# Kernel optimization log

Hardware: AMD Instinct MI355X
Metric: run time of the kernel (lower is better)

The kernel has to match this reference:

```python
import jax, jax.numpy as jnp
import numpy as np

B, CIN, H, W = 8, 64, 128, 128
COUT, K = 64, 3
STRIDE, PAD, DIL, G = 1, 1, 1, 1
T = K * K
HO = (H + 2 * PAD - (DIL * (K - 1) + 1)) // STRIDE + 1
WO = (W + 2 * PAD - (DIL * (K - 1) + 1)) // STRIDE + 1


def setup_inputs() -> dict:
    key = jax.random.key(0)
    ks = jax.random.split(key, 5)
    x = jax.random.normal(ks[0], (B, CIN, H, W), jnp.float32)
    offset = jax.random.normal(ks[1], (B, 2 * G * T, HO, WO), jnp.float32)
    mask = jax.random.uniform(ks[2], (B, G * T, HO, WO), jnp.float32)
    weight = jax.random.normal(ks[3], (COUT, CIN, K, K), jnp.float32) * (1.0 / np.sqrt(CIN * T))
    bias = jnp.zeros((COUT,), jnp.float32)
    return {"x": x, "offset": offset, "mask": mask, "weight": weight, "bias": bias}


def _gather(img_f, idx):
    # img_f: [Cg, H*W], idx: [T, Ho, Wo] -> [Cg, T, Ho, Wo]
    return img_f[:, idx]


def _dcn(x, offset, mask, weight, bias):
    Bn, Cin, Hh, Ww = x.shape
    Cout = weight.shape[0]
    Cg = Cin // G
    # offset channels laid out as [G, T, (dy, dx)] per DCNv2 convention
    off = offset.reshape(Bn, G, T, 2, HO, WO)
    dy, dx = off[:, :, :, 0], off[:, :, :, 1]  # [B, G, T, Ho, Wo]
    ky, kx = jnp.meshgrid(jnp.arange(K), jnp.arange(K), indexing="ij")
    ky = (ky.reshape(T) * DIL).astype(jnp.float32)
    kx = (kx.reshape(T) * DIL).astype(jnp.float32)
    base_y = (jnp.arange(HO) * STRIDE - PAD).astype(jnp.float32)
    base_x = (jnp.arange(WO) * STRIDE - PAD).astype(jnp.float32)
    # absolute sampling coordinates per (batch, def-group, tap, out-row, out-col)
    py = dy + base_y[None, None, None, :, None] + ky[None, None, :, None, None]
    px = dx + base_x[None, None, None, None, :] + kx[None, None, :, None, None]
    y0 = jnp.floor(py)
    x0 = jnp.floor(px)
    imgf = x.reshape(Bn, G, Cg, Hh * Ww)
    gather = jax.vmap(jax.vmap(_gather))  # over B and G
    sampled = jnp.zeros((Bn, G, Cg, T, HO, WO), x.dtype)
    # bilinear interpolation with zero padding outside the image
    for oy, ox in ((y0, x0), (y0, x0 + 1.0), (y0 + 1.0, x0), (y0 + 1.0, x0 + 1.0)):
        wgt = (1.0 - jnp.abs(py - oy)) * (1.0 - jnp.abs(px - ox))
        valid = (oy >= 0) & (oy < Hh) & (ox >= 0) & (ox < Ww)
        yi = jnp.clip(oy, 0, Hh - 1).astype(jnp.int32)
        xi = jnp.clip(ox, 0, Ww - 1).astype(jnp.int32)
        vals = gather(imgf, yi * Ww + xi)  # [B, G, Cg, T, Ho, Wo]
        sampled = sampled + vals * (wgt * valid)[:, :, None]
    # modulation mask, then accumulate taps into output channels
    m = mask.reshape(Bn, G, T, HO, WO)
    sampled = sampled * m[:, :, None]
    wr = weight.reshape(Cout, G, Cg, T)
    out = jnp.einsum("bgctij,ogct->boij", sampled, wr) + bias[None, :, None, None]
    return out


def reference(x, offset, mask, weight, bias):
    return _dcn(x, offset, mask, weight, bias)
```

## Files before the change

kernel.cpp:

```cpp
#include <hip/hip_runtime.h>
#include <stdint.h>

#define Bn   8
#define CIN  64
#define Hh   128
#define Wh   128
#define COUT 64
#define Tt   9
#define HO   128
#define WO   128
#define HW   (HO * WO)

#define RH     18
#define RWID   16
#define RREC   (RH * RWID)
#define HALO_Y 5
#define HALO_X 4

typedef _Float16 h16;
typedef __attribute__((ext_vector_type(2))) _Float16 h2;
typedef __attribute__((ext_vector_type(8))) _Float16 h8;
typedef __attribute__((ext_vector_type(4))) float   f4;

__device__ h16 g_xT[(size_t)Bn * Hh * Wh * CIN];
__device__ h16 g_wh[Tt * COUT * CIN];

__global__ __launch_bounds__(256) void prep(const float* __restrict__ x,
                                            const float* __restrict__ w) {
    if (blockIdx.x >= Bn * Hh) {
        int tid = (blockIdx.x - Bn * Hh) * 256 + threadIdx.x;
        int t   = tid >> 12;
        int rem = tid & 4095;
        int o   = rem >> 6;
        int c   = rem & 63;
        float v = w[(size_t)(o * 64 + c) * 9 + t];
        int ks = c >> 5, q = (c >> 3) & 3, j = c & 7;
        int mt = o >> 4, o15 = o & 15;
        g_wh[t * 4096 + ks * 2048 + mt * 512 + q * 128 + o15 * 8 + j] = (h16)v;
        return;
    }
    int b = blockIdx.x >> 7;
    int y = blockIdx.x & 127;
    __shared__ uint32_t tile[64][65];

    const float* src = x + ((size_t)b * CIN) * (Hh * Wh) + (size_t)y * Wh;
    int t    = threadIdx.x;
    int xp   = t & 63;
    int csub = t >> 6;
    #pragma unroll
    for (int cc = 0; cc < 64; cc += 4) {
        int c = cc + csub;
        float2 v = *(const float2*)(src + (size_t)c * (Hh * Wh) + xp * 2);
        uint32_t h0 = (uint32_t)__builtin_bit_cast(uint16_t, (h16)v.x);
        uint32_t h1 = (uint32_t)__builtin_bit_cast(uint16_t, (h16)v.y);
        tile[c][xp] = h0 | (h1 << 16);
    }
    __syncthreads();

    uint32_t* dst = (uint32_t*)(g_xT + (((size_t)b * Hh + y) * Wh) * CIN);
    int d  = t & 31;
    int xo = t >> 5;
    #pragma unroll
    for (int it = 0; it < 16; ++it) {
        int xg = it * 8 + xo;
        uint32_t lo = tile[2 * d][xg >> 1];
        uint32_t hi = tile[2 * d + 1][xg >> 1];
        int sh = (xg & 1) * 16;
        uint32_t l0 = (lo >> sh) & 0xffffu;
        uint32_t h1 = (hi >> sh) & 0xffffu;
        dst[xg * 32 + d] = l0 | (h1 << 16);
    }
}

__global__ __launch_bounds__(256) void dcn_main(
        const float* __restrict__ offset, const float* __restrict__ mask,
        const float* __restrict__ bias, float* __restrict__ out) {
    __shared__ __align__(16) uint8_t sreg[RREC * 128];

    int blk  = blockIdx.x;
    int b    = blk & 7;
    int s    = blk >> 3;
    int ty   = s >> 4, tx = s & 15;
    int i0   = ty * 8, j0 = tx * 8;
    int lane = threadIdx.x & 63;
    int wave = threadIdx.x >> 6;
    int n15  = lane & 15;
    int q    = lane >> 4;

    const h16* xb = g_xT + (size_t)b * (Hh * Wh * CIN);

    int i = i0 + (wave << 1) + (n15 >> 3);
    int j = j0 + (n15 & 7);
    int p = (i << 7) + j;

    const float* offB = offset + (size_t)b * (2 * Tt * HW);
    const float* mskB = mask   + (size_t)b * (Tt * HW);
    float dyv[Tt], dxv[Tt], mmv[Tt];
    #pragma unroll
    for (int t = 0; t < Tt; ++t) {
        dyv[t] = offB[(2 * t) * HW + p];
        dxv[t] = offB[(2 * t + 1) * HW + p];
        mmv[t] = mskB[t * HW + p];
    }

    {
        const int base_y = i0 - HALO_Y, base_x = j0 - HALO_X;
        #pragma unroll
        for (int it = 0; it < 9; ++it) {
            int idx  = it * 256 + threadIdx.x;
            int rec  = idx >> 3;
            int quad = idx & 7;
            int ry = rec >> 4, rx = rec & 15;
            int gy = min(max(base_y + ry, 0), Hh - 1);
            int gx = min(max(base_x + rx, 0), Wh - 1);
            uint4 v = *(const uint4*)(xb + ((gy << 7) + gx) * 64 + quad * 8);
            *(uint4*)(sreg + rec * 128 + ((quad ^ (rec & 7)) << 4)) = v;
        }
    }
    __syncthreads();

    f4 acc[4] = {{0.f,0.f,0.f,0.f},{0.f,0.f,0.f,0.f},
                 {0.f,0.f,0.f,0.f},{0.f,0.f,0.f,0.f}};

    #pragma unroll
    for (int t = 0; t < Tt; ++t) {
        const int ky = t / 3, kx = t % 3;
        float py = dyv[t] + (float)(i + ky - 1);
        float px = dxv[t] + (float)(j + kx - 1);
        float fy = floorf(py), fx = floorf(px);
        int   y0 = (int)fy,    x0 = (int)fx;
        float ly = py - fy,    lx = px - fx;
        float hy = 1.f - ly,   hx = 1.f - lx;

        bool vy0 = (y0 >= 0) && (y0 < Hh);
        bool vy1 = (y0 >= -1) && (y0 < Hh - 1);
        bool vx0 = (x0 >= 0) && (x0 < Wh);
        bool vx1 = (x0 >= -1) && (x0 < Wh - 1);
        float m = mmv[t];
        float w00 = (vy0 && vx0) ? hy * hx * m : 0.f;
        float w01 = (vy0 && vx1) ? hy * lx * m : 0.f;
        float w10 = (vy1 && vx0) ? ly * hx * m : 0.f;
        float w11 = (vy1 && vx1) ? ly * lx * m : 0.f;

        int ry = y0 - i0 + HALO_Y;
        int rx = x0 - j0 + HALO_X;
        bool intile = (ry >= 0) & (ry <= RH - 2) & (rx >= 0) & (rx <= RWID - 2);
        int ryc = min(max(ry, 0), RH - 2), rxc = min(max(rx, 0), RWID - 2);
        int pl00 = ryc * RWID + rxc;
        int pl01 = pl00 + 1, pl10 = pl00 + RWID, pl11 = pl00 + RWID + 1;

        union U4 { uint4 v; h2 h[4]; };
        U4 c00[2], c01[2], c10[2], c11[2];
        #pragma unroll
        for (int ks = 0; ks < 2; ++ks) {
            int qd = q + ks * 4;
            c00[ks].v = *(const uint4*)(sreg + pl00 * 128 + ((qd ^ (pl00 & 7)) << 4));
            c01[ks].v = *(const uint4*)(sreg + pl01 * 128 + ((qd ^ (pl01 & 7)) << 4));
            c10[ks].v = *(const uint4*)(sreg + pl10 * 128 + ((qd ^ (pl10 & 7)) << 4));
            c11[ks].v = *(const uint4*)(sreg + pl11 * 128 + ((qd ^ (pl11 & 7)) << 4));
        }
        if (__any(!intile)) {
            if (!intile) {
                int y0c = min(max(y0, 0), Hh - 1), y1c = min(max(y0 + 1, 0), Hh - 1);
                int x0c = min(max(x0, 0), Wh - 1), x1c = min(max(x0 + 1, 0), Wh - 1);
                const h16* r0 = xb + (size_t)(y0c * Wh) * CIN;
                const h16* r1 = xb + (size_t)(y1c * Wh) * CIN;
                #pragma unroll
                for (int ks = 0; ks < 2; ++ks) {
                    int c = q * 8 + ks * 32;
                    c00[ks].v = *(const uint4*)(r0 + x0c * CIN + c);
                    c01[ks].v = *(const uint4*)(r0 + x1c * CIN + c);
                    c10[ks].v = *(const uint4*)(r1 + x0c * CIN + c);
                    c11[ks].v = *(const uint4*)(r1 + x1c * CIN + c);
                }
            }
        }

        h2 W00 = {(h16)w00, (h16)w00};
        h2 W01 = {(h16)w01, (h16)w01};
        h2 W10 = {(h16)w10, (h16)w10};
        h2 W11 = {(h16)w11, (h16)w11};

        h8 bfrag[2];
        #pragma unroll
        for (int ks = 0; ks < 2; ++ks) {
            union { h2 r[4]; h8 v; } pk;
            #pragma unroll
            for (int e = 0; e < 4; ++e) {
                h2 r = c00[ks].h[e] * W00;
                r = c01[ks].h[e] * W01 + r;
                r = c10[ks].h[e] * W10 + r;
                r = c11[ks].h[e] * W11 + r;
                pk.r[e] = r;
            }
            bfrag[ks] = pk.v;
        }

        const h16* wt = g_wh + t * 4096;
        #pragma unroll
        for (int ks = 0; ks < 2; ++ks) {
            #pragma unroll
            for (int mt = 0; mt < 4; ++mt) {
                h8 a = *(const h8*)(wt + ks * 2048 + mt * 512 + lane * 8);
                acc[mt] = __builtin_amdgcn_mfma_f32_16x16x32_f16(
                    a, bfrag[ks], acc[mt], 0, 0, 0);
            }
        }
    }

    #pragma unroll
    for (int mt = 0; mt < 4; ++mt) {
        #pragma unroll
        for (int r = 0; r < 4; ++r) {
            int o = mt * 16 + q * 4 + r;
            out[(size_t)(b * COUT + o) * HW + p] = acc[mt][r] + bias[o];
        }
    }
}

extern "C" void kernel_launch(void* const* d_in, const int* in_sizes, int n_in,
                              void* d_out, int out_size, void* d_ws, size_t ws_size,
                              hipStream_t stream) {
    const float* x      = (const float*)d_in[0];
    const float* offset = (const float*)d_in[1];
    const float* mask   = (const float*)d_in[2];
    const float* weight = (const float*)d_in[3];
    const float* bias   = (const float*)d_in[4];
    (void)d_ws; (void)ws_size;

    prep<<<Bn * Hh + 144, 256, 0, stream>>>(x, weight);
    dcn_main<<<Bn * 256, 256, 0, stream>>>(offset, mask, bias, (float*)d_out);
}
```

Baseline: 129.5 us.

## Switch to 32x32x16 MFMA with wider 8x16 output tiles per block

Replaces the 16x16x32 MFMA tiles with 32x32x16 MFMA, so each wave covers 32 output pixels by 64 output channels in two accumulators. The weights are re-laid out in prep to match the new A-fragment layout. Block tiles widen from 8x8 to 8x16 pixels with a 19x25 shared-memory halo region, which halves the block count and lowers the halo-reload overhead per pixel. The cost is larger shared memory per block, fewer blocks to hide latency, and the bilinear interpolation done per lane over 4 k-slices instead of 2.

```diff
diff --git a/kernel.cpp b/kernel.cpp
--- a/kernel.cpp
+++ b/kernel.cpp
@@ -11,19 +11,19 @@
 #define WO   128
 #define HW   (HO * WO)
 
-#define RH     18
-#define RWID   16
-#define RREC   (RH * RWID)
+#define RH     19
+#define RWC    25
+#define RREC   (RH * RWC)
 #define HALO_Y 5
 #define HALO_X 4
 
 typedef _Float16 h16;
-typedef __attribute__((ext_vector_type(2))) _Float16 h2;
-typedef __attribute__((ext_vector_type(8))) _Float16 h8;
-typedef __attribute__((ext_vector_type(4))) float   f4;
+typedef __attribute__((ext_vector_type(2)))  _Float16 h2;
+typedef __attribute__((ext_vector_type(8)))  _Float16 h8;
+typedef __attribute__((ext_vector_type(16))) float    f16v;
 
 __device__ h16 g_xT[(size_t)Bn * Hh * Wh * CIN];
-__device__ h16 g_wh[Tt * COUT * CIN];
+__device__ h16 g_wh[Tt * 4 * 2 * 64 * 8];
 
 __global__ __launch_bounds__(256) void prep(const float* __restrict__ x,
                                             const float* __restrict__ w) {
@@ -31,12 +31,13 @@
         int tid = (blockIdx.x - Bn * Hh) * 256 + threadIdx.x;
         int t   = tid >> 12;
         int rem = tid & 4095;
-        int o   = rem >> 6;
-        int c   = rem & 63;
-        float v = w[(size_t)(o * 64 + c) * 9 + t];
-        int ks = c >> 5, q = (c >> 3) & 3, j = c & 7;
-        int mt = o >> 4, o15 = o & 15;
-        g_wh[t * 4096 + ks * 2048 + mt * 512 + q * 128 + o15 * 8 + j] = (h16)v;
+        int ks  = rem >> 10;
+        int mt  = (rem >> 9) & 1;
+        int ln  = (rem >> 3) & 63;
+        int j   = rem & 7;
+        int o   = mt * 32 + (ln & 31);
+        int c   = ks * 16 + ((ln >> 5) << 3) + j;
+        g_wh[tid] = (h16)w[(size_t)(o * 64 + c) * 9 + t];
         return;
     }
     int b = blockIdx.x >> 7;
@@ -80,17 +81,17 @@
     int blk  = blockIdx.x;
     int b    = blk & 7;
     int s    = blk >> 3;
-    int ty   = s >> 4, tx = s & 15;
-    int i0   = ty * 8, j0 = tx * 8;
+    int ty   = s >> 3, tx = s & 7;
+    int i0   = ty * 8, j0 = tx * 16;
     int lane = threadIdx.x & 63;
     int wave = threadIdx.x >> 6;
-    int n15  = lane & 15;
-    int q    = lane >> 4;
+    int n    = lane & 31;
+    int g    = lane >> 5;
 
     const h16* xb = g_xT + (size_t)b * (Hh * Wh * CIN);
 
-    int i = i0 + (wave << 1) + (n15 >> 3);
-    int j = j0 + (n15 & 7);
+    int i = i0 + 2 * wave + (n >> 4);
+    int j = j0 + (n & 15);
     int p = (i << 7) + j;
 
     const float* offB = offset + (size_t)b * (2 * Tt * HW);
@@ -106,21 +107,22 @@
     {
         const int base_y = i0 - HALO_Y, base_x = j0 - HALO_X;
         #pragma unroll
-        for (int it = 0; it < 9; ++it) {
+        for (int it = 0; it < 15; ++it) {
             int idx  = it * 256 + threadIdx.x;
             int rec  = idx >> 3;
             int quad = idx & 7;
-            int ry = rec >> 4, rx = rec & 15;
-            int gy = min(max(base_y + ry, 0), Hh - 1);
-            int gx = min(max(base_x + rx, 0), Wh - 1);
-            uint4 v = *(const uint4*)(xb + ((gy << 7) + gx) * 64 + quad * 8);
-            *(uint4*)(sreg + rec * 128 + ((quad ^ (rec & 7)) << 4)) = v;
+            if (rec < RREC) {
+                int ry = rec / RWC, rx = rec - ry * RWC;
+                int gy = min(max(base_y + ry, 0), Hh - 1);
+                int gx = min(max(base_x + rx, 0), Wh - 1);
+                uint4 v = *(const uint4*)(xb + ((gy << 7) + gx) * 64 + quad * 8);
+                *(uint4*)(sreg + rec * 128 + ((quad ^ (rec & 7)) << 4)) = v;
+            }
         }
     }
     __syncthreads();
 
-    f4 acc[4] = {{0.f,0.f,0.f,0.f},{0.f,0.f,0.f,0.f},
-                 {0.f,0.f,0.f,0.f},{0.f,0.f,0.f,0.f}};
+    f16v acc[2] = {};
 
     #pragma unroll
     for (int t = 0; t < Tt; ++t) {
@@ -144,16 +146,16 @@
 
         int ry = y0 - i0 + HALO_Y;
         int rx = x0 - j0 + HALO_X;
-        bool intile = (ry >= 0) & (ry <= RH - 2) & (rx >= 0) & (rx <= RWID - 2);
-        int ryc = min(max(ry, 0), RH - 2), rxc = min(max(rx, 0), RWID - 2);
-        int pl00 = ryc * RWID + rxc;
-        int pl01 = pl00 + 1, pl10 = pl00 + RWID, pl11 = pl00 + RWID + 1;
+        bool intile = (ry >= 0) & (ry <= RH - 2) & (rx >= 0) & (rx <= RWC - 2);
+        int ryc = min(max(ry, 0), RH - 2), rxc = min(max(rx, 0), RWC - 2);
+        int pl00 = ryc * RWC + rxc;
+        int pl01 = pl00 + 1, pl10 = pl00 + RWC, pl11 = pl00 + RWC + 1;
 
         union U4 { uint4 v; h2 h[4]; };
-        U4 c00[2], c01[2], c10[2], c11[2];
-        #pragma unroll
-        for (int ks = 0; ks < 2; ++ks) {
-            int qd = q + ks * 4;
+        U4 c00[4], c01[4], c10[4], c11[4];
+        #pragma unroll
+        for (int ks = 0; ks < 4; ++ks) {
+            int qd = ks * 2 + g;
             c00[ks].v = *(const uint4*)(sreg + pl00 * 128 + ((qd ^ (pl00 & 7)) << 4));
             c01[ks].v = *(const uint4*)(sreg + pl01 * 128 + ((qd ^ (pl01 & 7)) << 4));
             c10[ks].v = *(const uint4*)(sreg + pl10 * 128 + ((qd ^ (pl10 & 7)) << 4));
@@ -166,8 +168,8 @@
                 const h16* r0 = xb + (size_t)(y0c * Wh) * CIN;
                 const h16* r1 = xb + (size_t)(y1c * Wh) * CIN;
                 #pragma unroll
-                for (int ks = 0; ks < 2; ++ks) {
-                    int c = q * 8 + ks * 32;
+                for (int ks = 0; ks < 4; ++ks) {
+                    int c = ks * 16 + g * 8;
                     c00[ks].v = *(const uint4*)(r0 + x0c * CIN + c);
                     c01[ks].v = *(const uint4*)(r0 + x1c * CIN + c);
                     c10[ks].v = *(const uint4*)(r1 + x0c * CIN + c);
@@ -181,9 +183,9 @@
         h2 W10 = {(h16)w10, (h16)w10};
         h2 W11 = {(h16)w11, (h16)w11};
 
-        h8 bfrag[2];
-        #pragma unroll
-        for (int ks = 0; ks < 2; ++ks) {
+        const h16* wt = g_wh + t * 4096;
+        #pragma unroll
+        for (int ks = 0; ks < 4; ++ks) {
             union { h2 r[4]; h8 v; } pk;
             #pragma unroll
             for (int e = 0; e < 4; ++e) {
@@ -193,26 +195,20 @@
                 r = c11[ks].h[e] * W11 + r;
                 pk.r[e] = r;
             }
-            bfrag[ks] = pk.v;
-        }
-
-        const h16* wt = g_wh + t * 4096;
-        #pragma unroll
-        for (int ks = 0; ks < 2; ++ks) {
             #pragma unroll
-            for (int mt = 0; mt < 4; ++mt) {
-                h8 a = *(const h8*)(wt + ks * 2048 + mt * 512 + lane * 8);
-                acc[mt] = __builtin_amdgcn_mfma_f32_16x16x32_f16(
-                    a, bfrag[ks], acc[mt], 0, 0, 0);
-            }
-        }
-    }
-
-    #pragma unroll
-    for (int mt = 0; mt < 4; ++mt) {
-        #pragma unroll
-        for (int r = 0; r < 4; ++r) {
-            int o = mt * 16 + q * 4 + r;
+            for (int mt = 0; mt < 2; ++mt) {
+                h8 a = *(const h8*)(wt + (ks * 2 + mt) * 512 + lane * 8);
+                acc[mt] = __builtin_amdgcn_mfma_f32_32x32x16_f16(
+                    a, pk.v, acc[mt], 0, 0, 0);
+            }
+        }
+    }
+
+    #pragma unroll
+    for (int mt = 0; mt < 2; ++mt) {
+        #pragma unroll
+        for (int r = 0; r < 16; ++r) {
+            int o = mt * 32 + (r & 3) + 8 * (r >> 2) + 4 * g;
             out[(size_t)(b * COUT + o) * HW + p] = acc[mt][r] + bias[o];
         }
     }
@@ -229,5 +225,5 @@
     (void)d_ws; (void)ws_size;
 
     prep<<<Bn * Hh + 144, 256, 0, stream>>>(x, weight);
-    dcn_main<<<Bn * 256, 256, 0, stream>>>(offset, mask, bias, (float*)d_out);
+    dcn_main<<<Bn * 128, 256, 0, stream>>>(offset, mask, bias, (float*)d_out);
 }
```

New measurement: 122.3 us. 1.06x faster.
